# Performance work log

Measured on AMD Instinct MI355X. Metric: run time of the kernel, lower is better.

Reference implementation:

```python
import jax, jax.numpy as jnp
import numpy as np

SEQ_LEN = 2048
EMBED_DIM = 1024
NUM_HEADS = 16
DIM_HEAD = EMBED_DIM // NUM_HEADS
BATCH = 4


def setup_inputs() -> dict:
    key = jax.random.key(0)
    k1, k2, k3 = jax.random.split(key, 3)
    x = jax.random.normal(k1, (SEQ_LEN, BATCH, EMBED_DIM), dtype=jnp.float32)
    weight_qkv = jax.random.normal(k2, (3 * EMBED_DIM, EMBED_DIM), dtype=jnp.float32) * (EMBED_DIM ** -0.5)
    weight_out = jax.random.normal(k3, (EMBED_DIM, EMBED_DIM), dtype=jnp.float32) * (EMBED_DIM ** -0.5)
    # causal mask: True where attention is DISALLOWED (strict upper triangle)
    mask = ~jnp.tril(jnp.ones((SEQ_LEN, SEQ_LEN), dtype=bool))[None, None]  # [1,1,L,L]
    return {"x": x, "weight_qkv": weight_qkv, "weight_out": weight_out, "mask": mask}


def reference(x, weight_qkv, weight_out, mask):
    L, N, E = x.shape
    H, Dh = NUM_HEADS, DIM_HEAD
    scale = Dh ** -0.5
    qkv = x @ weight_qkv.T                       # [L, N, 3E]
    q, k, v = jnp.split(qkv, 3, axis=-1)         # each [L, N, E]
    # [L, N, E] -> [N*H, L, Dh]
    def to_heads(t):
        return t.reshape(L, N * H, Dh).transpose(1, 0, 2)
    q, k, v = to_heads(q) * scale, to_heads(k), to_heads(v)
    attn = jnp.einsum('bld,bmd->blm', q, k)      # [N*H, L, L]
    attn = attn.reshape(N, H, L, L)
    attn = jnp.where(mask, jnp.float32(-100000.0), attn)
    attn = jax.nn.softmax(attn.reshape(N * H, L, L), axis=-1)
    out = jnp.einsum('blm,bmd->bld', attn, v)    # [N*H, L, Dh]
    out = out.transpose(1, 0, 2).reshape(L, N, E)
    return out @ weight_out.T
```

## Files before the change

kernel.cpp:

```cpp
#include <hip/hip_runtime.h>
#include <hip/hip_bf16.h>
#include <stdint.h>

constexpr int L  = 2048;
constexpr int NB = 4;
constexpr int E  = 1024;
constexpr int H  = 16;
constexpr int M  = L * NB;
constexpr int K  = E;
constexpr int QKV_LD = 3 * E;

typedef float  f32x4  __attribute__((ext_vector_type(4)));
typedef float  f32x16 __attribute__((ext_vector_type(16)));
typedef __bf16 bf16x4 __attribute__((ext_vector_type(4)));
typedef __bf16 bf16x8 __attribute__((ext_vector_type(8)));
typedef unsigned int uint2v __attribute__((ext_vector_type(2)));
typedef unsigned int uint4v __attribute__((ext_vector_type(4)));

#define AS1 __attribute__((address_space(1)))
#define AS3 __attribute__((address_space(3)))

static __device__ __forceinline__ void gl_lds16(const void* g, void* l) {
  __builtin_amdgcn_global_load_lds((const AS1 uint32_t*)g, (AS3 uint32_t*)l, 16, 0, 0);
}

__global__ __launch_bounds__(256)
void cvt_all(const float* __restrict__ x, const float* __restrict__ wq,
             const float* __restrict__ wo, __bf16* __restrict__ xb,
             __bf16* __restrict__ wqb, __bf16* __restrict__ wob) {
  const int bid = blockIdx.x;
  const float* src;
  __bf16* dst;
  int i;
  if (bid < 8192)        { src = x;  dst = xb;  i = bid * 256 + threadIdx.x; }
  else if (bid < 11264)  { src = wq; dst = wqb; i = (bid - 8192) * 256 + threadIdx.x; }
  else                   { src = wo; dst = wob; i = (bid - 11264) * 256 + threadIdx.x; }
  const f32x4 v = ((const f32x4*)src)[i];
  bf16x4 o;
#pragma unroll
  for (int j = 0; j < 4; j++) o[j] = (__bf16)v[j];
  ((bf16x4*)dst)[i] = o;
}

template<int NC, typename OutT>
__global__ __launch_bounds__(256)
void gemm_bt(const __bf16* __restrict__ A, const __bf16* __restrict__ B,
             OutT* __restrict__ C) {
  constexpr int BK = 64;
  __shared__ char lds[2 * 128 * BK * 2];
  char* aL = lds;
  char* bL = lds + 128 * BK * 2;

  const int t    = threadIdx.x;
  const int lane = t & 63;
  const int w    = t >> 6;
  const int g    = lane >> 4;
  const int c    = lane & 15;

  const int nwg = gridDim.x * gridDim.y;
  const int lin = blockIdx.x + gridDim.x * blockIdx.y;
  const int q8  = nwg >> 3;
  const int swz = (lin & 7) * q8 + (lin >> 3);
  const int bx  = swz % gridDim.x;
  const int by  = swz / gridDim.x;

  const int rowBase = by * 128;
  const int colBase = bx * 128;

  const int srow = t >> 3;
  const int scb  = (t & 7) * 16;
  const int ssw  = scb ^ ((srow & 7) << 4);

  const char* aSrcBase = (const char*)(A + (size_t)(rowBase + srow) * K) + ssw;
  const char* bSrcBase = (const char*)(B + (size_t)(colBase + srow) * K) + ssw;

  f32x4 acc[4][4];
#pragma unroll
  for (int i = 0; i < 4; i++)
#pragma unroll
    for (int j = 0; j < 4; j++) acc[i][j] = f32x4{0.f, 0.f, 0.f, 0.f};

  const int wr = (w >> 1) * 64;
  const int wc = (w & 1) * 64;

  for (int k0 = 0; k0 < K; k0 += BK) {
    __syncthreads();
#pragma unroll
    for (int q = 0; q < 4; q++) {
      gl_lds16(aSrcBase + (size_t)2 * k0 + (size_t)q * 32 * K * 2, aL + q * 4096 + t * 16);
      gl_lds16(bSrcBase + (size_t)2 * k0 + (size_t)q * 32 * K * 2, bL + q * 4096 + t * 16);
    }
    __syncthreads();

    bf16x8 af[4][2], bfR[4][2];
#pragma unroll
    for (int mi = 0; mi < 4; mi++) {
      const int row = wr + mi * 16 + c;
      const int sw  = (row & 7) << 4;
#pragma unroll
      for (int ks = 0; ks < 2; ks++)
        af[mi][ks] = *(const bf16x8*)(aL + row * 128 + ((ks * 64 + g * 16) ^ sw));
    }
#pragma unroll
    for (int ni = 0; ni < 4; ni++) {
      const int row = wc + ni * 16 + c;
      const int sw  = (row & 7) << 4;
#pragma unroll
      for (int ks = 0; ks < 2; ks++)
        bfR[ni][ks] = *(const bf16x8*)(bL + row * 128 + ((ks * 64 + g * 16) ^ sw));
    }
#pragma unroll
    for (int mi = 0; mi < 4; mi++)
#pragma unroll
      for (int ni = 0; ni < 4; ni++)
#pragma unroll
        for (int ks = 0; ks < 2; ks++)
          acc[mi][ni] = __builtin_amdgcn_mfma_f32_16x16x32_bf16(
              af[mi][ks], bfR[ni][ks], acc[mi][ni], 0, 0, 0);
  }

#pragma unroll
  for (int mi = 0; mi < 4; mi++)
#pragma unroll
    for (int ni = 0; ni < 4; ni++)
#pragma unroll
      for (int r = 0; r < 4; r++) {
        const int row = rowBase + wr + mi * 16 + g * 4 + r;
        const int col = colBase + wc + ni * 16 + c;
        C[(size_t)row * NC + col] = (OutT)acc[mi][ni][r];
      }
}

__global__ __launch_bounds__(256)
void transpose_v(const __bf16* __restrict__ qkv, __bf16* __restrict__ vT) {
  __shared__ char tile[64 * 160];
  const int lt = blockIdx.x;
  const int bh = blockIdx.y;
  const int n  = bh >> 4, h = bh & 15;
  const int t  = threadIdx.x;
  const int r8 = t >> 3;
  const int c8 = (t & 7) * 8;

#pragma unroll
  for (int q2 = 0; q2 < 2; q2++) {
    const int l = q2 * 32 + r8;
    const bf16x8 v = *(const bf16x8*)(qkv + (size_t)((lt * 64 + l) * 4 + n) * QKV_LD +
                                      2 * E + h * 64 + c8);
    *(bf16x8*)(tile + l * 160 + ((c8 * 2) ^ (((l >> 3) & 7) << 4))) = v;
  }
  __syncthreads();
#pragma unroll
  for (int q2 = 0; q2 < 2; q2++) {
    const int d = q2 * 32 + r8;
    bf16x8 o;
#pragma unroll
    for (int i = 0; i < 8; i++) {
      const int l = c8 + i;
      o[i] = *(const __bf16*)(tile + l * 160 + ((d * 2) ^ (((l >> 3) & 7) << 4)));
    }
    *(bf16x8*)(vT + ((size_t)bh * 64 + d) * 2048 + lt * 64 + c8) = o;
  }
}

__global__ __launch_bounds__(256)
void attn_kernel(const __bf16* __restrict__ qkv, const __bf16* __restrict__ vT,
                 __bf16* __restrict__ out) {
  const int b  = blockIdx.x;
  const int y  = blockIdx.y;
  const int n  = b >> 4;
  const int h  = b & 15;

  __shared__ char kl[2][64 * 128];
  __shared__ char vl[2][64 * 128];

  const int t    = threadIdx.x;
  const int lane = t & 63;
  const int w    = t >> 6;
  const int l31  = lane & 31;
  const int hi   = lane >> 5;

  const int srow = t >> 3;
  const int scb  = (t & 7) * 16;
  int kssw[2];
#pragma unroll
  for (int q2 = 0; q2 < 2; q2++) {
    const int row = q2 * 32 + srow;
    kssw[q2] = scb ^ (((row ^ (row >> 3)) & 7) << 4);
  }

  const int krow0 = l31,      sw0 = ((krow0 ^ (krow0 >> 3)) & 7) << 4;
  const int krow1 = 32 + l31, sw1 = ((krow1 ^ (krow1 >> 3)) & 7) << 4;

  constexpr float QSCALE = 0.125f * 1.4426950408889634f;

  int cur = 0;

#pragma unroll
  for (int q2 = 0; q2 < 2; q2++) {
    const int kvrow = q2 * 32 + srow;
    gl_lds16((const char*)(qkv + (size_t)(kvrow * 4 + n) * QKV_LD + E + h * 64) + kssw[q2],
             kl[0] + q2 * 4096 + t * 16);
    gl_lds16((const char*)(vT + ((size_t)b * 64 + kvrow) * 2048) + kssw[q2],
             vl[0] + q2 * 4096 + t * 16);
  }

  for (int pass = 0; pass < 2; ++pass) {
    const int qsup = pass ? 15 - y : y;
    const int qb_  = qsup * 128 + w * 32;
    const int qg   = qb_ + l31;
    const int ktEnd = 2 * qsup + 1;

    bf16x8 qb[4];
    {
      const __bf16* qp = qkv + (size_t)(qg * 4 + n) * QKV_LD + h * 64;
#pragma unroll
      for (int ds = 0; ds < 4; ds++) {
        qb[ds] = *(const bf16x8*)(qp + ds * 16 + hi * 8);
#pragma unroll
        for (int i = 0; i < 8; i++) qb[ds][i] = (__bf16)((float)qb[ds][i] * QSCALE);
      }
    }

    float m_c = -3e38f, l_c = 0.f;
    f32x16 o0, o1;
#pragma unroll
    for (int j = 0; j < 16; j++) { o0[j] = 0.f; o1[j] = 0.f; }

    for (int kt = 0; kt <= ktEnd; ++kt) {
      __syncthreads();

      const bool last = (kt == ktEnd);
      if (!last || pass == 0) {
        const int nx = last ? 0 : kt + 1;
#pragma unroll
        for (int q2 = 0; q2 < 2; q2++) {
          const int kvrow = nx * 64 + q2 * 32 + srow;
          gl_lds16((const char*)(qkv + (size_t)(kvrow * 4 + n) * QKV_LD + E + h * 64) + kssw[q2],
                   kl[cur ^ 1] + q2 * 4096 + t * 16);
          const int vd = q2 * 32 + srow;
          gl_lds16((const char*)(vT + ((size_t)b * 64 + vd) * 2048 + nx * 64) + kssw[q2],
                   vl[cur ^ 1] + q2 * 4096 + t * 16);
        }
      }
      __builtin_amdgcn_sched_barrier(0);

      if (kt * 64 <= qb_ + 31) {
        const char* klc = kl[cur];
        const char* vlc = vl[cur];

        f32x16 s0, s1;
#pragma unroll
        for (int j = 0; j < 16; j++) { s0[j] = 0.f; s1[j] = 0.f; }
        __builtin_amdgcn_s_setprio(1);
#pragma unroll
        for (int ds = 0; ds < 4; ds++) {
          const int col = ds * 32 + hi * 16;
          const bf16x8 ka0 = *(const bf16x8*)(klc + krow0 * 128 + (col ^ sw0));
          const bf16x8 ka1 = *(const bf16x8*)(klc + krow1 * 128 + (col ^ sw1));
          s0 = __builtin_amdgcn_mfma_f32_32x32x16_bf16(ka0, qb[ds], s0, 0, 0, 0);
          s1 = __builtin_amdgcn_mfma_f32_32x32x16_bf16(ka1, qb[ds], s1, 0, 0, 0);
        }
        __builtin_amdgcn_s_setprio(0);

        if (kt * 64 + 63 > qb_) {
#pragma unroll
          for (int reg = 0; reg < 16; reg++) {
            const int kvp = (reg & 3) + 8 * (reg >> 2) + 4 * hi;
            if (kt * 64 + kvp      > qg) s0[reg] = -1e30f;
            if (kt * 64 + 32 + kvp > qg) s1[reg] = -1e30f;
          }
        }

        float rmax = s0[0];
#pragma unroll
        for (int reg = 1; reg < 16; reg++) rmax = fmaxf(rmax, s0[reg]);
#pragma unroll
        for (int reg = 0; reg < 16; reg++) rmax = fmaxf(rmax, s1[reg]);
        rmax = fmaxf(rmax, __shfl_xor(rmax, 32));

        if (__any(rmax > m_c + 8.f)) {
          const float mnew  = fmaxf(m_c, rmax);
          const float alpha = exp2f(m_c - mnew);
          l_c *= alpha;
#pragma unroll
          for (int reg = 0; reg < 16; reg++) {
            const int   qp = (reg & 3) + 8 * (reg >> 2) + 4 * hi;
            const float ar = __shfl(alpha, qp);
            o0[reg] *= ar;
            o1[reg] *= ar;
          }
          m_c = mnew;
        }

        float rsum = 0.f;
#pragma unroll
        for (int reg = 0; reg < 16; reg++) {
          const float e0 = exp2f(s0[reg] - m_c);
          const float e1 = exp2f(s1[reg] - m_c);
          s0[reg] = e0; s1[reg] = e1;
          rsum += e0 + e1;
        }
        rsum += __shfl_xor(rsum, 32);
        l_c += rsum;

        unsigned int runA[8], runB[8];
#pragma unroll
        for (int rg = 0; rg < 8; rg++) {
          bf16x4 pk;
#pragma unroll
          for (int j = 0; j < 4; j++)
            pk[j] = (__bf16)((rg < 4) ? s0[(rg & 3) * 4 + j] : s1[(rg & 3) * 4 + j]);
          const uint2v u = *(const uint2v*)&pk;
          runA[rg] = u[0]; runB[rg] = u[1];
        }

#pragma unroll
        for (int s_ = 0; s_ < 4; s_++) {
          const unsigned int ownA = hi ? runA[2 * s_ + 1] : runA[2 * s_];
          const unsigned int ownB = hi ? runB[2 * s_ + 1] : runB[2 * s_];
          const unsigned int sndA = hi ? runA[2 * s_]     : runA[2 * s_ + 1];
          const unsigned int sndB = hi ? runB[2 * s_]     : runB[2 * s_ + 1];
          const unsigned int rxA  = (unsigned int)__shfl_xor((int)sndA, 32);
          const unsigned int rxB  = (unsigned int)__shfl_xor((int)sndB, 32);
          uint4v pu;
          pu[0] = hi ? rxA : ownA;  pu[1] = hi ? rxB : ownB;
          pu[2] = hi ? ownA : rxA;  pu[3] = hi ? ownB : rxB;
          const bf16x8 pa = *(const bf16x8*)&pu;

          const int colp = s_ * 32 + hi * 16;
          const bf16x8 vb0 = *(const bf16x8*)(vlc + krow0 * 128 + (colp ^ sw0));
          const bf16x8 vb1 = *(const bf16x8*)(vlc + krow1 * 128 + (colp ^ sw1));
          __builtin_amdgcn_s_setprio(1);
          o0 = __builtin_amdgcn_mfma_f32_32x32x16_bf16(pa, vb0, o0, 0, 0, 0);
          o1 = __builtin_amdgcn_mfma_f32_32x32x16_bf16(pa, vb1, o1, 0, 0, 0);
          __builtin_amdgcn_s_setprio(0);
        }
      }

      cur ^= 1;
    }

    const float inv = 1.f / l_c;
#pragma unroll
    for (int reg = 0; reg < 16; reg++) {
      const int   qp  = (reg & 3) + 8 * (reg >> 2) + 4 * hi;
      const float li  = __shfl(inv, qp);
      const int   qrw = qb_ + qp;
      const size_t base = (size_t)(qrw * 4 + n) * E + h * 64;
      out[base + l31]      = (__bf16)(o0[reg] * li);
      out[base + 32 + l31] = (__bf16)(o1[reg] * li);
    }
  }
}

extern "C" void kernel_launch(void* const* d_in, const int* in_sizes, int n_in,
                              void* d_out, int out_size, void* d_ws, size_t ws_size,
                              hipStream_t stream) {
  const float* x    = (const float*)d_in[0];
  const float* wqkv = (const float*)d_in[1];
  const float* wout = (const float*)d_in[2];

  char* ws = (char*)d_ws;
  __bf16* x_bf    = (__bf16*)ws;                         ws += (size_t)M * E * 2;
  __bf16* wqkv_bf = (__bf16*)ws;                         ws += (size_t)QKV_LD * E * 2;
  __bf16* wout_bf = (__bf16*)ws;                         ws += (size_t)E * E * 2;
  __bf16* qkv     = (__bf16*)ws;                         ws += (size_t)M * QKV_LD * 2;
  __bf16* attno   = (__bf16*)ws;
  __bf16* vT      = x_bf;
  float*  outp    = (float*)d_out;

  cvt_all<<<12288, 256, 0, stream>>>(x, wqkv, wout, x_bf, wqkv_bf, wout_bf);

  gemm_bt<QKV_LD, __bf16><<<dim3(QKV_LD / 128, M / 128), 256, 0, stream>>>(x_bf, wqkv_bf, qkv);
  transpose_v<<<dim3(L / 64, NB * H), 256, 0, stream>>>(qkv, vT);
  attn_kernel<<<dim3(NB * H, 8), 256, 0, stream>>>(qkv, vT, attno);
  gemm_bt<E, float><<<dim3(E / 128, M / 128), 256, 0, stream>>>(attno, wout_bf, outp);
}
```

Before: 193.9 us.

## Split attention KV range across two warp groups with LDS merge of partial softmax

The attention block grows to 512 threads, forming two 4-wave groups that each cover part of the combined 34 KV-tile workload of the paired query blocks, 17 tiles per group. Group 1 finishes part of the long query block, saves its partial O, m and l to shared memory, then switches to the short block. Group 0 merges those partial results at the end. This balances work inside a block and doubles waves per block, but drops the double-buffered async prefetch in favour of load-then-sync each step. It also stores the partial O in bf16, which slightly reduces precision.

```diff
diff --git a/kernel.cpp b/kernel.cpp
--- a/kernel.cpp
+++ b/kernel.cpp
@@ -162,7 +162,7 @@
   }
 }
 
-__global__ __launch_bounds__(256)
+__global__ __launch_bounds__(512)
 void attn_kernel(const __bf16* __restrict__ qkv, const __bf16* __restrict__ vT,
                  __bf16* __restrict__ out) {
   const int b  = blockIdx.x;
@@ -170,17 +170,22 @@
   const int n  = b >> 4;
   const int h  = b & 15;
 
-  __shared__ char kl[2][64 * 128];
-  __shared__ char vl[2][64 * 128];
+  __shared__ char   kb[2][64 * 128];
+  __shared__ char   vb[2][64 * 128];
+  __shared__ __bf16 mO[128 * 64];
+  __shared__ float  mML[128 * 2];
 
   const int t    = threadIdx.x;
   const int lane = t & 63;
   const int w    = t >> 6;
+  const int wg   = w >> 2;
+  const int wl   = w & 3;
   const int l31  = lane & 31;
   const int hi   = lane >> 5;
 
-  const int srow = t >> 3;
-  const int scb  = (t & 7) * 16;
+  const int tg   = t & 255;
+  const int srow = tg >> 3;
+  const int scb  = (tg & 7) * 16;
   int kssw[2];
 #pragma unroll
   for (int q2 = 0; q2 < 2; q2++) {
@@ -193,153 +198,169 @@
 
   constexpr float QSCALE = 0.125f * 1.4426950408889634f;
 
-  int cur = 0;
-
-#pragma unroll
-  for (int q2 = 0; q2 < 2; q2++) {
-    const int kvrow = q2 * 32 + srow;
-    gl_lds16((const char*)(qkv + (size_t)(kvrow * 4 + n) * QKV_LD + E + h * 64) + kssw[q2],
-             kl[0] + q2 * 4096 + t * 16);
-    gl_lds16((const char*)(vT + ((size_t)b * 64 + kvrow) * 2048) + kssw[q2],
-             vl[0] + q2 * 4096 + t * 16);
-  }
-
-  for (int pass = 0; pass < 2; ++pass) {
-    const int qsup = pass ? 15 - y : y;
-    const int qb_  = qsup * 128 + w * 32;
-    const int qg   = qb_ + l31;
-    const int ktEnd = 2 * qsup + 1;
-
-    bf16x8 qb[4];
-    {
+  const int sS = y, sL = 15 - y;
+  const int jSwitch = 15 - 2 * y;
+
+  char* kls = kb[wg];
+  char* vls = vb[wg];
+
+  int qb_ = sL * 128 + wl * 32;
+  int qg  = qb_ + l31;
+
+  bf16x8 qf[4];
+  {
+    const __bf16* qp = qkv + (size_t)(qg * 4 + n) * QKV_LD + h * 64;
+#pragma unroll
+    for (int ds = 0; ds < 4; ds++) {
+      qf[ds] = *(const bf16x8*)(qp + ds * 16 + hi * 8);
+#pragma unroll
+      for (int i = 0; i < 8; i++) qf[ds][i] = (__bf16)((float)qf[ds][i] * QSCALE);
+    }
+  }
+
+  float m_c = -3e38f, l_c = 0.f;
+  f32x16 o0, o1;
+#pragma unroll
+  for (int j = 0; j < 16; j++) { o0[j] = 0.f; o1[j] = 0.f; }
+
+  for (int j = 0; j < 17; ++j) {
+    int kt;
+    if (wg == 0)            kt = j;
+    else if (j < jSwitch)   kt = 17 + j;
+    else                    kt = j - jSwitch;
+
+    if (wg == 1 && j == jSwitch) {
+#pragma unroll
+      for (int reg = 0; reg < 16; reg++) {
+        const int qp  = (reg & 3) + 8 * (reg >> 2) + 4 * hi;
+        const int row = wl * 32 + qp;
+        mO[row * 64 + l31]      = (__bf16)o0[reg];
+        mO[row * 64 + 32 + l31] = (__bf16)o1[reg];
+      }
+      if (hi == 0) {
+        mML[(wl * 32 + l31) * 2]     = m_c;
+        mML[(wl * 32 + l31) * 2 + 1] = l_c;
+      }
+      m_c = -3e38f; l_c = 0.f;
+#pragma unroll
+      for (int jj = 0; jj < 16; jj++) { o0[jj] = 0.f; o1[jj] = 0.f; }
+      qb_ = sS * 128 + wl * 32;
+      qg  = qb_ + l31;
       const __bf16* qp = qkv + (size_t)(qg * 4 + n) * QKV_LD + h * 64;
 #pragma unroll
       for (int ds = 0; ds < 4; ds++) {
-        qb[ds] = *(const bf16x8*)(qp + ds * 16 + hi * 8);
-#pragma unroll
-        for (int i = 0; i < 8; i++) qb[ds][i] = (__bf16)((float)qb[ds][i] * QSCALE);
-      }
-    }
-
-    float m_c = -3e38f, l_c = 0.f;
-    f32x16 o0, o1;
-#pragma unroll
-    for (int j = 0; j < 16; j++) { o0[j] = 0.f; o1[j] = 0.f; }
-
-    for (int kt = 0; kt <= ktEnd; ++kt) {
-      __syncthreads();
-
-      const bool last = (kt == ktEnd);
-      if (!last || pass == 0) {
-        const int nx = last ? 0 : kt + 1;
-#pragma unroll
-        for (int q2 = 0; q2 < 2; q2++) {
-          const int kvrow = nx * 64 + q2 * 32 + srow;
-          gl_lds16((const char*)(qkv + (size_t)(kvrow * 4 + n) * QKV_LD + E + h * 64) + kssw[q2],
-                   kl[cur ^ 1] + q2 * 4096 + t * 16);
-          const int vd = q2 * 32 + srow;
-          gl_lds16((const char*)(vT + ((size_t)b * 64 + vd) * 2048 + nx * 64) + kssw[q2],
-                   vl[cur ^ 1] + q2 * 4096 + t * 16);
+        qf[ds] = *(const bf16x8*)(qp + ds * 16 + hi * 8);
+#pragma unroll
+        for (int i = 0; i < 8; i++) qf[ds][i] = (__bf16)((float)qf[ds][i] * QSCALE);
+      }
+    }
+
+    __syncthreads();
+#pragma unroll
+    for (int q2 = 0; q2 < 2; q2++) {
+      const int kvrow = kt * 64 + q2 * 32 + srow;
+      gl_lds16((const char*)(qkv + (size_t)(kvrow * 4 + n) * QKV_LD + E + h * 64) + kssw[q2],
+               kls + q2 * 4096 + tg * 16);
+      const int vd = q2 * 32 + srow;
+      gl_lds16((const char*)(vT + ((size_t)b * 64 + vd) * 2048 + kt * 64) + kssw[q2],
+               vls + q2 * 4096 + tg * 16);
+    }
+    __syncthreads();
+
+    if (kt * 64 <= qb_ + 31) {
+      f32x16 s0, s1;
+#pragma unroll
+      for (int jj = 0; jj < 16; jj++) { s0[jj] = 0.f; s1[jj] = 0.f; }
+      __builtin_amdgcn_s_setprio(1);
+#pragma unroll
+      for (int ds = 0; ds < 4; ds++) {
+        const int col = ds * 32 + hi * 16;
+        const bf16x8 ka0 = *(const bf16x8*)(kls + krow0 * 128 + (col ^ sw0));
+        const bf16x8 ka1 = *(const bf16x8*)(kls + krow1 * 128 + (col ^ sw1));
+        s0 = __builtin_amdgcn_mfma_f32_32x32x16_bf16(ka0, qf[ds], s0, 0, 0, 0);
+        s1 = __builtin_amdgcn_mfma_f32_32x32x16_bf16(ka1, qf[ds], s1, 0, 0, 0);
+      }
+      __builtin_amdgcn_s_setprio(0);
+
+      if (kt * 64 + 63 > qb_) {
+#pragma unroll
+        for (int reg = 0; reg < 16; reg++) {
+          const int kvp = (reg & 3) + 8 * (reg >> 2) + 4 * hi;
+          if (kt * 64 + kvp      > qg) s0[reg] = -1e30f;
+          if (kt * 64 + 32 + kvp > qg) s1[reg] = -1e30f;
         }
       }
-      __builtin_amdgcn_sched_barrier(0);
-
-      if (kt * 64 <= qb_ + 31) {
-        const char* klc = kl[cur];
-        const char* vlc = vl[cur];
-
-        f32x16 s0, s1;
-#pragma unroll
-        for (int j = 0; j < 16; j++) { s0[j] = 0.f; s1[j] = 0.f; }
+
+      float rmax = s0[0];
+#pragma unroll
+      for (int reg = 1; reg < 16; reg++) rmax = fmaxf(rmax, s0[reg]);
+#pragma unroll
+      for (int reg = 0; reg < 16; reg++) rmax = fmaxf(rmax, s1[reg]);
+      rmax = fmaxf(rmax, __shfl_xor(rmax, 32));
+
+      if (__any(rmax > m_c + 8.f)) {
+        const float mnew  = fmaxf(m_c, rmax);
+        const float alpha = exp2f(m_c - mnew);
+        l_c *= alpha;
+#pragma unroll
+        for (int reg = 0; reg < 16; reg++) {
+          const int   qp = (reg & 3) + 8 * (reg >> 2) + 4 * hi;
+          const float ar = __shfl(alpha, qp);
+          o0[reg] *= ar;
+          o1[reg] *= ar;
+        }
+        m_c = mnew;
+      }
+
+      float rsum = 0.f;
+#pragma unroll
+      for (int reg = 0; reg < 16; reg++) {
+        const float e0 = exp2f(s0[reg] - m_c);
+        const float e1 = exp2f(s1[reg] - m_c);
+        s0[reg] = e0; s1[reg] = e1;
+        rsum += e0 + e1;
+      }
+      rsum += __shfl_xor(rsum, 32);
+      l_c += rsum;
+
+      unsigned int runA[8], runB[8];
+#pragma unroll
+      for (int rg = 0; rg < 8; rg++) {
+        bf16x4 pk;
+#pragma unroll
+        for (int jj = 0; jj < 4; jj++)
+          pk[jj] = (__bf16)((rg < 4) ? s0[(rg & 3) * 4 + jj] : s1[(rg & 3) * 4 + jj]);
+        const uint2v u = *(const uint2v*)&pk;
+        runA[rg] = u[0]; runB[rg] = u[1];
+      }
+
+#pragma unroll
+      for (int s_ = 0; s_ < 4; s_++) {
+        const unsigned int ownA = hi ? runA[2 * s_ + 1] : runA[2 * s_];
+        const unsigned int ownB = hi ? runB[2 * s_ + 1] : runB[2 * s_];
+        const unsigned int sndA = hi ? runA[2 * s_]     : runA[2 * s_ + 1];
+        const unsigned int sndB = hi ? runB[2 * s_]     : runB[2 * s_ + 1];
+        const unsigned int rxA  = (unsigned int)__shfl_xor((int)sndA, 32);
+        const unsigned int rxB  = (unsigned int)__shfl_xor((int)sndB, 32);
+        uint4v pu;
+        pu[0] = hi ? rxA : ownA;  pu[1] = hi ? rxB : ownB;
+        pu[2] = hi ? ownA : rxA;  pu[3] = hi ? ownB : rxB;
+        const bf16x8 pa = *(const bf16x8*)&pu;
+
+        const int colp = s_ * 32 + hi * 16;
+        const bf16x8 vb0 = *(const bf16x8*)(vls + krow0 * 128 + (colp ^ sw0));
+        const bf16x8 vb1 = *(const bf16x8*)(vls + krow1 * 128 + (colp ^ sw1));
         __builtin_amdgcn_s_setprio(1);
-#pragma unroll
-        for (int ds = 0; ds < 4; ds++) {
-          const int col = ds * 32 + hi * 16;
-          const bf16x8 ka0 = *(const bf16x8*)(klc + krow0 * 128 + (col ^ sw0));
-          const bf16x8 ka1 = *(const bf16x8*)(klc + krow1 * 128 + (col ^ sw1));
-          s0 = __builtin_amdgcn_mfma_f32_32x32x16_bf16(ka0, qb[ds], s0, 0, 0, 0);
-          s1 = __builtin_amdgcn_mfma_f32_32x32x16_bf16(ka1, qb[ds], s1, 0, 0, 0);
-        }
+        o0 = __builtin_amdgcn_mfma_f32_32x32x16_bf16(pa, vb0, o0, 0, 0, 0);
+        o1 = __builtin_amdgcn_mfma_f32_32x32x16_bf16(pa, vb1, o1, 0, 0, 0);
         __builtin_amdgcn_s_setprio(0);
-
-        if (kt * 64 + 63 > qb_) {
-#pragma unroll
-          for (int reg = 0; reg < 16; reg++) {
-            const int kvp = (reg & 3) + 8 * (reg >> 2) + 4 * hi;
-            if (kt * 64 + kvp      > qg) s0[reg] = -1e30f;
-            if (kt * 64 + 32 + kvp > qg) s1[reg] = -1e30f;
-          }
-        }
-
-        float rmax = s0[0];
-#pragma unroll
-        for (int reg = 1; reg < 16; reg++) rmax = fmaxf(rmax, s0[reg]);
-#pragma unroll
-        for (int reg = 0; reg < 16; reg++) rmax = fmaxf(rmax, s1[reg]);
-        rmax = fmaxf(rmax, __shfl_xor(rmax, 32));
-
-        if (__any(rmax > m_c + 8.f)) {
-          const float mnew  = fmaxf(m_c, rmax);
-          const float alpha = exp2f(m_c - mnew);
-          l_c *= alpha;
-#pragma unroll
-          for (int reg = 0; reg < 16; reg++) {
-            const int   qp = (reg & 3) + 8 * (reg >> 2) + 4 * hi;
-            const float ar = __shfl(alpha, qp);
-            o0[reg] *= ar;
-            o1[reg] *= ar;
-          }
-          m_c = mnew;
-        }
-
-        float rsum = 0.f;
-#pragma unroll
-        for (int reg = 0; reg < 16; reg++) {
-          const float e0 = exp2f(s0[reg] - m_c);
-          const float e1 = exp2f(s1[reg] - m_c);
-          s0[reg] = e0; s1[reg] = e1;
-          rsum += e0 + e1;
-        }
-        rsum += __shfl_xor(rsum, 32);
-        l_c += rsum;
-
-        unsigned int runA[8], runB[8];
-#pragma unroll
-        for (int rg = 0; rg < 8; rg++) {
-          bf16x4 pk;
-#pragma unroll
-          for (int j = 0; j < 4; j++)
-            pk[j] = (__bf16)((rg < 4) ? s0[(rg & 3) * 4 + j] : s1[(rg & 3) * 4 + j]);
-          const uint2v u = *(const uint2v*)&pk;
-          runA[rg] = u[0]; runB[rg] = u[1];
-        }
-
-#pragma unroll
-        for (int s_ = 0; s_ < 4; s_++) {
-          const unsigned int ownA = hi ? runA[2 * s_ + 1] : runA[2 * s_];
-          const unsigned int ownB = hi ? runB[2 * s_ + 1] : runB[2 * s_];
-          const unsigned int sndA = hi ? runA[2 * s_]     : runA[2 * s_ + 1];
-          const unsigned int sndB = hi ? runB[2 * s_]     : runB[2 * s_ + 1];
-          const unsigned int rxA  = (unsigned int)__shfl_xor((int)sndA, 32);
-          const unsigned int rxB  = (unsigned int)__shfl_xor((int)sndB, 32);
-          uint4v pu;
-          pu[0] = hi ? rxA : ownA;  pu[1] = hi ? rxB : ownB;
-          pu[2] = hi ? ownA : rxA;  pu[3] = hi ? ownB : rxB;
-          const bf16x8 pa = *(const bf16x8*)&pu;
-
-          const int colp = s_ * 32 + hi * 16;
-          const bf16x8 vb0 = *(const bf16x8*)(vlc + krow0 * 128 + (colp ^ sw0));
-          const bf16x8 vb1 = *(const bf16x8*)(vlc + krow1 * 128 + (colp ^ sw1));
-          __builtin_amdgcn_s_setprio(1);
-          o0 = __builtin_amdgcn_mfma_f32_32x32x16_bf16(pa, vb0, o0, 0, 0, 0);
-          o1 = __builtin_amdgcn_mfma_f32_32x32x16_bf16(pa, vb1, o1, 0, 0, 0);
-          __builtin_amdgcn_s_setprio(0);
-        }
-      }
-
-      cur ^= 1;
-    }
-
+      }
+    }
+  }
+
+  __syncthreads();
+
+  if (wg == 1) {
     const float inv = 1.f / l_c;
 #pragma unroll
     for (int reg = 0; reg < 16; reg++) {
@@ -349,6 +370,30 @@
       const size_t base = (size_t)(qrw * 4 + n) * E + h * 64;
       out[base + l31]      = (__bf16)(o0[reg] * li);
       out[base + 32 + l31] = (__bf16)(o1[reg] * li);
+    }
+  } else {
+    const float mB = mML[(wl * 32 + l31) * 2];
+    const float lB = mML[(wl * 32 + l31) * 2 + 1];
+    const float mF = fmaxf(m_c, mB);
+    const float aA = exp2f(m_c - mF);
+    const float aB = exp2f(mB - mF);
+    const float lF = l_c * aA + lB * aB;
+    const float iv = 1.f / lF;
+#pragma unroll
+    for (int reg = 0; reg < 16; reg++) {
+      const int   qp  = (reg & 3) + 8 * (reg >> 2) + 4 * hi;
+      const float aAr = __shfl(aA, qp);
+      const float aBr = __shfl(aB, qp);
+      const float ivr = __shfl(iv, qp);
+      const int   row = wl * 32 + qp;
+      const float b0  = (float)mO[row * 64 + l31];
+      const float b1  = (float)mO[row * 64 + 32 + l31];
+      const float v0  = (o0[reg] * aAr + b0 * aBr) * ivr;
+      const float v1  = (o1[reg] * aAr + b1 * aBr) * ivr;
+      const int   qrw = qb_ + qp;
+      const size_t base = (size_t)(qrw * 4 + n) * E + h * 64;
+      out[base + l31]      = (__bf16)v0;
+      out[base + 32 + l31] = (__bf16)v1;
     }
   }
 }
@@ -373,6 +418,6 @@
 
   gemm_bt<QKV_LD, __bf16><<<dim3(QKV_LD / 128, M / 128), 256, 0, stream>>>(x_bf, wqkv_bf, qkv);
   transpose_v<<<dim3(L / 64, NB * H), 256, 0, stream>>>(qkv, vT);
-  attn_kernel<<<dim3(NB * H, 8), 256, 0, stream>>>(qkv, vT, attno);
+  attn_kernel<<<dim3(NB * H, 8), 512, 0, stream>>>(qkv, vT, attno);
   gemm_bt<E, float><<<dim3(E / 128, M / 128), 256, 0, stream>>>(attno, wout_bf, outp);
 }
```

New measurement: 197.8 us. No clear change (+2.0%).

## Double KV tile size to 128 in causal attention kernel

Applied to the files above, without the earlier changes.

The attention kernel now processes 128 keys/values per iteration instead of 64, using four score accumulators per wave and a wider V tile with matching swizzles. This halves the number of loop iterations and barriers and amortizes softmax bookkeeping, but doubles LDS usage and register pressure. It also drops the per-wave skip of fully masked tiles, so on the diagonal tile some waves compute fully masked blocks.

```diff
diff --git a/kernel.cpp b/kernel.cpp
--- a/kernel.cpp
+++ b/kernel.cpp
@@ -170,8 +170,8 @@
   const int n  = b >> 4;
   const int h  = b & 15;
 
-  __shared__ char kl[2][64 * 128];
-  __shared__ char vl[2][64 * 128];
+  __shared__ char kl[2][128 * 128];
+  __shared__ char vl[2][64 * 256];
 
   const int t    = threadIdx.x;
   const int lane = t & 63;
@@ -179,28 +179,44 @@
   const int l31  = lane & 31;
   const int hi   = lane >> 5;
 
-  const int srow = t >> 3;
-  const int scb  = (t & 7) * 16;
-  int kssw[2];
-#pragma unroll
-  for (int q2 = 0; q2 < 2; q2++) {
-    const int row = q2 * 32 + srow;
-    kssw[q2] = scb ^ (((row ^ (row >> 3)) & 7) << 4);
-  }
-
-  const int krow0 = l31,      sw0 = ((krow0 ^ (krow0 >> 3)) & 7) << 4;
-  const int krow1 = 32 + l31, sw1 = ((krow1 ^ (krow1 >> 3)) & 7) << 4;
+  const int srowK = t >> 3;
+  const int scbK  = (t & 7) * 16;
+  int sswK[4];
+#pragma unroll
+  for (int q2 = 0; q2 < 4; q2++) {
+    const int row = q2 * 32 + srowK;
+    sswK[q2] = scbK ^ (((row ^ (row >> 3)) & 7) << 4);
+  }
+  const int srowV = t >> 4;
+  const int scbV  = (t & 15) * 16;
+  int sswV[4];
+#pragma unroll
+  for (int q2 = 0; q2 < 4; q2++) {
+    const int row = q2 * 16 + srowV;
+    sswV[q2] = scbV ^ (((row ^ (row >> 3)) & 7) << 4);
+  }
+
+  int ksw[4];
+#pragma unroll
+  for (int j = 0; j < 4; j++) {
+    const int row = j * 32 + l31;
+    ksw[j] = ((row ^ (row >> 3)) & 7) << 4;
+  }
+  const int vsw0 = ((l31 ^ (l31 >> 3)) & 7) << 4;
+  const int vrow1 = 32 + l31;
+  const int vsw1 = ((vrow1 ^ (vrow1 >> 3)) & 7) << 4;
 
   constexpr float QSCALE = 0.125f * 1.4426950408889634f;
 
   int cur = 0;
 
 #pragma unroll
-  for (int q2 = 0; q2 < 2; q2++) {
-    const int kvrow = q2 * 32 + srow;
-    gl_lds16((const char*)(qkv + (size_t)(kvrow * 4 + n) * QKV_LD + E + h * 64) + kssw[q2],
+  for (int q2 = 0; q2 < 4; q2++) {
+    const int kvrow = q2 * 32 + srowK;
+    gl_lds16((const char*)(qkv + (size_t)(kvrow * 4 + n) * QKV_LD + E + h * 64) + sswK[q2],
              kl[0] + q2 * 4096 + t * 16);
-    gl_lds16((const char*)(vT + ((size_t)b * 64 + kvrow) * 2048) + kssw[q2],
+    const int vd = q2 * 16 + srowV;
+    gl_lds16((const char*)(vT + ((size_t)b * 64 + vd) * 2048) + sswV[q2],
              vl[0] + q2 * 4096 + t * 16);
   }
 
@@ -208,7 +224,7 @@
     const int qsup = pass ? 15 - y : y;
     const int qb_  = qsup * 128 + w * 32;
     const int qg   = qb_ + l31;
-    const int ktEnd = 2 * qsup + 1;
+    const int ktEnd = qsup;
 
     bf16x8 qb[4];
     {
@@ -233,108 +249,129 @@
       if (!last || pass == 0) {
         const int nx = last ? 0 : kt + 1;
 #pragma unroll
-        for (int q2 = 0; q2 < 2; q2++) {
-          const int kvrow = nx * 64 + q2 * 32 + srow;
-          gl_lds16((const char*)(qkv + (size_t)(kvrow * 4 + n) * QKV_LD + E + h * 64) + kssw[q2],
+        for (int q2 = 0; q2 < 4; q2++) {
+          const int kvrow = nx * 128 + q2 * 32 + srowK;
+          gl_lds16((const char*)(qkv + (size_t)(kvrow * 4 + n) * QKV_LD + E + h * 64) + sswK[q2],
                    kl[cur ^ 1] + q2 * 4096 + t * 16);
-          const int vd = q2 * 32 + srow;
-          gl_lds16((const char*)(vT + ((size_t)b * 64 + vd) * 2048 + nx * 64) + kssw[q2],
+          const int vd = q2 * 16 + srowV;
+          gl_lds16((const char*)(vT + ((size_t)b * 64 + vd) * 2048 + nx * 128) + sswV[q2],
                    vl[cur ^ 1] + q2 * 4096 + t * 16);
         }
       }
       __builtin_amdgcn_sched_barrier(0);
 
-      if (kt * 64 <= qb_ + 31) {
-        const char* klc = kl[cur];
-        const char* vlc = vl[cur];
-
-        f32x16 s0, s1;
-#pragma unroll
-        for (int j = 0; j < 16; j++) { s0[j] = 0.f; s1[j] = 0.f; }
+      const char* klc = kl[cur];
+      const char* vlc = vl[cur];
+
+      f32x16 s0, s1, s2, s3;
+#pragma unroll
+      for (int j = 0; j < 16; j++) { s0[j] = 0.f; s1[j] = 0.f; s2[j] = 0.f; s3[j] = 0.f; }
+      __builtin_amdgcn_s_setprio(1);
+#pragma unroll
+      for (int ds = 0; ds < 4; ds++) {
+        const int col = ds * 32 + hi * 16;
+        const bf16x8 ka0 = *(const bf16x8*)(klc + (0 * 32 + l31) * 128 + (col ^ ksw[0]));
+        const bf16x8 ka1 = *(const bf16x8*)(klc + (1 * 32 + l31) * 128 + (col ^ ksw[1]));
+        const bf16x8 ka2 = *(const bf16x8*)(klc + (2 * 32 + l31) * 128 + (col ^ ksw[2]));
+        const bf16x8 ka3 = *(const bf16x8*)(klc + (3 * 32 + l31) * 128 + (col ^ ksw[3]));
+        s0 = __builtin_amdgcn_mfma_f32_32x32x16_bf16(ka0, qb[ds], s0, 0, 0, 0);
+        s1 = __builtin_amdgcn_mfma_f32_32x32x16_bf16(ka1, qb[ds], s1, 0, 0, 0);
+        s2 = __builtin_amdgcn_mfma_f32_32x32x16_bf16(ka2, qb[ds], s2, 0, 0, 0);
+        s3 = __builtin_amdgcn_mfma_f32_32x32x16_bf16(ka3, qb[ds], s3, 0, 0, 0);
+      }
+      __builtin_amdgcn_s_setprio(0);
+
+      if (last) {
+#pragma unroll
+        for (int reg = 0; reg < 16; reg++) {
+          const int kvp = (reg & 3) + 8 * (reg >> 2) + 4 * hi;
+          const int kb0 = kt * 128 + kvp;
+          if (kb0      > qg) s0[reg] = -1e30f;
+          if (kb0 + 32 > qg) s1[reg] = -1e30f;
+          if (kb0 + 64 > qg) s2[reg] = -1e30f;
+          if (kb0 + 96 > qg) s3[reg] = -1e30f;
+        }
+      }
+
+      float rmax = s0[0];
+#pragma unroll
+      for (int reg = 1; reg < 16; reg++) rmax = fmaxf(rmax, s0[reg]);
+#pragma unroll
+      for (int reg = 0; reg < 16; reg++) rmax = fmaxf(rmax, s1[reg]);
+#pragma unroll
+      for (int reg = 0; reg < 16; reg++) rmax = fmaxf(rmax, s2[reg]);
+#pragma unroll
+      for (int reg = 0; reg < 16; reg++) rmax = fmaxf(rmax, s3[reg]);
+      rmax = fmaxf(rmax, __shfl_xor(rmax, 32));
+
+      if (__any(rmax > m_c + 8.f)) {
+        const float mnew  = fmaxf(m_c, rmax);
+        const float alpha = exp2f(m_c - mnew);
+        l_c *= alpha;
+#pragma unroll
+        for (int reg = 0; reg < 16; reg++) {
+          const int   qp = (reg & 3) + 8 * (reg >> 2) + 4 * hi;
+          const float ar = __shfl(alpha, qp);
+          o0[reg] *= ar;
+          o1[reg] *= ar;
+        }
+        m_c = mnew;
+      }
+
+      float rsum = 0.f;
+#pragma unroll
+      for (int reg = 0; reg < 16; reg++) {
+        const float e0 = exp2f(s0[reg] - m_c);
+        const float e1 = exp2f(s1[reg] - m_c);
+        const float e2 = exp2f(s2[reg] - m_c);
+        const float e3 = exp2f(s3[reg] - m_c);
+        s0[reg] = e0; s1[reg] = e1; s2[reg] = e2; s3[reg] = e3;
+        rsum += (e0 + e1) + (e2 + e3);
+      }
+      rsum += __shfl_xor(rsum, 32);
+      l_c += rsum;
+
+      unsigned int runA[16], runB[16];
+#pragma unroll
+      for (int f = 0; f < 4; f++)
+#pragma unroll
+        for (int rg = 0; rg < 4; rg++) {
+          bf16x4 pk;
+#pragma unroll
+          for (int j = 0; j < 4; j++) {
+            const int r = rg * 4 + j;
+            float v;
+            if      (f == 0) v = s0[r];
+            else if (f == 1) v = s1[r];
+            else if (f == 2) v = s2[r];
+            else             v = s3[r];
+            pk[j] = (__bf16)v;
+          }
+          const uint2v u = *(const uint2v*)&pk;
+          runA[f * 4 + rg] = u[0]; runB[f * 4 + rg] = u[1];
+        }
+
+#pragma unroll
+      for (int s_ = 0; s_ < 8; s_++) {
+        const int rg0 = (s_ >> 1) * 4 + 2 * (s_ & 1);
+        const unsigned int ownA = hi ? runA[rg0 + 1] : runA[rg0];
+        const unsigned int ownB = hi ? runB[rg0 + 1] : runB[rg0];
+        const unsigned int sndA = hi ? runA[rg0]     : runA[rg0 + 1];
+        const unsigned int sndB = hi ? runB[rg0]     : runB[rg0 + 1];
+        const unsigned int rxA  = (unsigned int)__shfl_xor((int)sndA, 32);
+        const unsigned int rxB  = (unsigned int)__shfl_xor((int)sndB, 32);
+        uint4v pu;
+        pu[0] = hi ? rxA : ownA;  pu[1] = hi ? rxB : ownB;
+        pu[2] = hi ? ownA : rxA;  pu[3] = hi ? ownB : rxB;
+        const bf16x8 pa = *(const bf16x8*)&pu;
+
+        const int colp = s_ * 32 + hi * 16;
+        const bf16x8 vb0 = *(const bf16x8*)(vlc + l31 * 256 + (colp ^ vsw0));
+        const bf16x8 vb1 = *(const bf16x8*)(vlc + vrow1 * 256 + (colp ^ vsw1));
         __builtin_amdgcn_s_setprio(1);
-#pragma unroll
-        for (int ds = 0; ds < 4; ds++) {
-          const int col = ds * 32 + hi * 16;
-          const bf16x8 ka0 = *(const bf16x8*)(klc + krow0 * 128 + (col ^ sw0));
-          const bf16x8 ka1 = *(const bf16x8*)(klc + krow1 * 128 + (col ^ sw1));
-          s0 = __builtin_amdgcn_mfma_f32_32x32x16_bf16(ka0, qb[ds], s0, 0, 0, 0);
-          s1 = __builtin_amdgcn_mfma_f32_32x32x16_bf16(ka1, qb[ds], s1, 0, 0, 0);
-        }
+        o0 = __builtin_amdgcn_mfma_f32_32x32x16_bf16(pa, vb0, o0, 0, 0, 0);
+        o1 = __builtin_amdgcn_mfma_f32_32x32x16_bf16(pa, vb1, o1, 0, 0, 0);
         __builtin_amdgcn_s_setprio(0);
-
-        if (kt * 64 + 63 > qb_) {
-#pragma unroll
-          for (int reg = 0; reg < 16; reg++) {
-            const int kvp = (reg & 3) + 8 * (reg >> 2) + 4 * hi;
-            if (kt * 64 + kvp      > qg) s0[reg] = -1e30f;
-            if (kt * 64 + 32 + kvp > qg) s1[reg] = -1e30f;
-          }
-        }
-
-        float rmax = s0[0];
-#pragma unroll
-        for (int reg = 1; reg < 16; reg++) rmax = fmaxf(rmax, s0[reg]);
-#pragma unroll
-        for (int reg = 0; reg < 16; reg++) rmax = fmaxf(rmax, s1[reg]);
-        rmax = fmaxf(rmax, __shfl_xor(rmax, 32));
-
-        if (__any(rmax > m_c + 8.f)) {
-          const float mnew  = fmaxf(m_c, rmax);
-          const float alpha = exp2f(m_c - mnew);
-          l_c *= alpha;
-#pragma unroll
-          for (int reg = 0; reg < 16; reg++) {
-            const int   qp = (reg & 3) + 8 * (reg >> 2) + 4 * hi;
-            const float ar = __shfl(alpha, qp);
-            o0[reg] *= ar;
-            o1[reg] *= ar;
-          }
-          m_c = mnew;
-        }
-
-        float rsum = 0.f;
-#pragma unroll
-        for (int reg = 0; reg < 16; reg++) {
-          const float e0 = exp2f(s0[reg] - m_c);
-          const float e1 = exp2f(s1[reg] - m_c);
-          s0[reg] = e0; s1[reg] = e1;
-          rsum += e0 + e1;
-        }
-        rsum += __shfl_xor(rsum, 32);
-        l_c += rsum;
-
-        unsigned int runA[8], runB[8];
-#pragma unroll
-        for (int rg = 0; rg < 8; rg++) {
-          bf16x4 pk;
-#pragma unroll
-          for (int j = 0; j < 4; j++)
-            pk[j] = (__bf16)((rg < 4) ? s0[(rg & 3) * 4 + j] : s1[(rg & 3) * 4 + j]);
-          const uint2v u = *(const uint2v*)&pk;
-          runA[rg] = u[0]; runB[rg] = u[1];
-        }
-
-#pragma unroll
-        for (int s_ = 0; s_ < 4; s_++) {
-          const unsigned int ownA = hi ? runA[2 * s_ + 1] : runA[2 * s_];
-          const unsigned int ownB = hi ? runB[2 * s_ + 1] : runB[2 * s_];
-          const unsigned int sndA = hi ? runA[2 * s_]     : runA[2 * s_ + 1];
-          const unsigned int sndB = hi ? runB[2 * s_]     : runB[2 * s_ + 1];
-          const unsigned int rxA  = (unsigned int)__shfl_xor((int)sndA, 32);
-          const unsigned int rxB  = (unsigned int)__shfl_xor((int)sndB, 32);
-          uint4v pu;
-          pu[0] = hi ? rxA : ownA;  pu[1] = hi ? rxB : ownB;
-          pu[2] = hi ? ownA : rxA;  pu[3] = hi ? ownB : rxB;
-          const bf16x8 pa = *(const bf16x8*)&pu;
-
-          const int colp = s_ * 32 + hi * 16;
-          const bf16x8 vb0 = *(const bf16x8*)(vlc + krow0 * 128 + (colp ^ sw0));
-          const bf16x8 vb1 = *(const bf16x8*)(vlc + krow1 * 128 + (colp ^ sw1));
-          __builtin_amdgcn_s_setprio(1);
-          o0 = __builtin_amdgcn_mfma_f32_32x32x16_bf16(pa, vb0, o0, 0, 0, 0);
-          o1 = __builtin_amdgcn_mfma_f32_32x32x16_bf16(pa, vb1, o1, 0, 0, 0);
-          __builtin_amdgcn_s_setprio(0);
-        }
       }
 
       cur ^= 1;
```

After: 214.3 us. +10.5%, slower.

## Split attention into 64-row query blocks with 2 waves, drop double-buffering

Applied to the files above, without the earlier changes.

Restructures the attention kernel from 8 blocks per head (256 threads, 128-row query tiles, paired light/heavy passes for causal balance) into 32 blocks per head of 128 threads, each handling a single 64-row query tile. The grid is launched heaviest-first so long causal rows start early. K/V tiles are now loaded single-buffered with a sync on each side instead of being prefetched into a double buffer. The aim is more blocks and occupancy on the GPU and less shared memory per block. The cost is exposed load latency on every tile and K/V reloaded by more blocks.

```diff
diff --git a/kernel.cpp b/kernel.cpp
--- a/kernel.cpp
+++ b/kernel.cpp
@@ -162,16 +162,16 @@
   }
 }
 
-__global__ __launch_bounds__(256)
+__global__ __launch_bounds__(128)
 void attn_kernel(const __bf16* __restrict__ qkv, const __bf16* __restrict__ vT,
                  __bf16* __restrict__ out) {
-  const int b  = blockIdx.x;
-  const int y  = blockIdx.y;
-  const int n  = b >> 4;
-  const int h  = b & 15;
-
-  __shared__ char kl[2][64 * 128];
-  __shared__ char vl[2][64 * 128];
+  const int b   = blockIdx.x;
+  const int sup = 31 - (int)blockIdx.y;
+  const int n   = b >> 4;
+  const int h   = b & 15;
+
+  __shared__ char kl[64 * 128];
+  __shared__ char vl[64 * 128];
 
   const int t    = threadIdx.x;
   const int lane = t & 63;
@@ -181,10 +181,10 @@
 
   const int srow = t >> 3;
   const int scb  = (t & 7) * 16;
-  int kssw[2];
-#pragma unroll
-  for (int q2 = 0; q2 < 2; q2++) {
-    const int row = q2 * 32 + srow;
+  int kssw[4];
+#pragma unroll
+  for (int q2 = 0; q2 < 4; q2++) {
+    const int row = q2 * 16 + srow;
     kssw[q2] = scb ^ (((row ^ (row >> 3)) & 7) << 4);
   }
 
@@ -193,163 +193,136 @@
 
   constexpr float QSCALE = 0.125f * 1.4426950408889634f;
 
-  int cur = 0;
-
-#pragma unroll
-  for (int q2 = 0; q2 < 2; q2++) {
-    const int kvrow = q2 * 32 + srow;
-    gl_lds16((const char*)(qkv + (size_t)(kvrow * 4 + n) * QKV_LD + E + h * 64) + kssw[q2],
-             kl[0] + q2 * 4096 + t * 16);
-    gl_lds16((const char*)(vT + ((size_t)b * 64 + kvrow) * 2048) + kssw[q2],
-             vl[0] + q2 * 4096 + t * 16);
-  }
-
-  for (int pass = 0; pass < 2; ++pass) {
-    const int qsup = pass ? 15 - y : y;
-    const int qb_  = qsup * 128 + w * 32;
-    const int qg   = qb_ + l31;
-    const int ktEnd = 2 * qsup + 1;
-
-    bf16x8 qb[4];
-    {
-      const __bf16* qp = qkv + (size_t)(qg * 4 + n) * QKV_LD + h * 64;
-#pragma unroll
-      for (int ds = 0; ds < 4; ds++) {
-        qb[ds] = *(const bf16x8*)(qp + ds * 16 + hi * 8);
-#pragma unroll
-        for (int i = 0; i < 8; i++) qb[ds][i] = (__bf16)((float)qb[ds][i] * QSCALE);
+  const int qb_ = sup * 64 + w * 32;
+  const int qg  = qb_ + l31;
+
+  bf16x8 qb[4];
+  {
+    const __bf16* qp = qkv + (size_t)(qg * 4 + n) * QKV_LD + h * 64;
+#pragma unroll
+    for (int ds = 0; ds < 4; ds++) {
+      qb[ds] = *(const bf16x8*)(qp + ds * 16 + hi * 8);
+#pragma unroll
+      for (int i = 0; i < 8; i++) qb[ds][i] = (__bf16)((float)qb[ds][i] * QSCALE);
+    }
+  }
+
+  float m_c = -3e38f, l_c = 0.f;
+  f32x16 o0, o1;
+#pragma unroll
+  for (int j = 0; j < 16; j++) { o0[j] = 0.f; o1[j] = 0.f; }
+
+  for (int kt = 0; kt <= sup; ++kt) {
+    __syncthreads();
+#pragma unroll
+    for (int q2 = 0; q2 < 4; q2++) {
+      const int kvrow = kt * 64 + q2 * 16 + srow;
+      gl_lds16((const char*)(qkv + (size_t)(kvrow * 4 + n) * QKV_LD + E + h * 64) + kssw[q2],
+               kl + q2 * 2048 + t * 16);
+      const int vd = q2 * 16 + srow;
+      gl_lds16((const char*)(vT + ((size_t)b * 64 + vd) * 2048 + kt * 64) + kssw[q2],
+               vl + q2 * 2048 + t * 16);
+    }
+    __syncthreads();
+
+    f32x16 s0, s1;
+#pragma unroll
+    for (int j = 0; j < 16; j++) { s0[j] = 0.f; s1[j] = 0.f; }
+    __builtin_amdgcn_s_setprio(1);
+#pragma unroll
+    for (int ds = 0; ds < 4; ds++) {
+      const int col = ds * 32 + hi * 16;
+      const bf16x8 ka0 = *(const bf16x8*)(kl + krow0 * 128 + (col ^ sw0));
+      const bf16x8 ka1 = *(const bf16x8*)(kl + krow1 * 128 + (col ^ sw1));
+      s0 = __builtin_amdgcn_mfma_f32_32x32x16_bf16(ka0, qb[ds], s0, 0, 0, 0);
+      s1 = __builtin_amdgcn_mfma_f32_32x32x16_bf16(ka1, qb[ds], s1, 0, 0, 0);
+    }
+    __builtin_amdgcn_s_setprio(0);
+
+    if (kt == sup) {
+#pragma unroll
+      for (int reg = 0; reg < 16; reg++) {
+        const int kvp = (reg & 3) + 8 * (reg >> 2) + 4 * hi;
+        if (kt * 64 + kvp      > qg) s0[reg] = -1e30f;
+        if (kt * 64 + 32 + kvp > qg) s1[reg] = -1e30f;
       }
     }
 
-    float m_c = -3e38f, l_c = 0.f;
-    f32x16 o0, o1;
-#pragma unroll
-    for (int j = 0; j < 16; j++) { o0[j] = 0.f; o1[j] = 0.f; }
-
-    for (int kt = 0; kt <= ktEnd; ++kt) {
-      __syncthreads();
-
-      const bool last = (kt == ktEnd);
-      if (!last || pass == 0) {
-        const int nx = last ? 0 : kt + 1;
-#pragma unroll
-        for (int q2 = 0; q2 < 2; q2++) {
-          const int kvrow = nx * 64 + q2 * 32 + srow;
-          gl_lds16((const char*)(qkv + (size_t)(kvrow * 4 + n) * QKV_LD + E + h * 64) + kssw[q2],
-                   kl[cur ^ 1] + q2 * 4096 + t * 16);
-          const int vd = q2 * 32 + srow;
-          gl_lds16((const char*)(vT + ((size_t)b * 64 + vd) * 2048 + nx * 64) + kssw[q2],
-                   vl[cur ^ 1] + q2 * 4096 + t * 16);
-        }
+    float rmax = s0[0];
+#pragma unroll
+    for (int reg = 1; reg < 16; reg++) rmax = fmaxf(rmax, s0[reg]);
+#pragma unroll
+    for (int reg = 0; reg < 16; reg++) rmax = fmaxf(rmax, s1[reg]);
+    rmax = fmaxf(rmax, __shfl_xor(rmax, 32));
+
+    if (__any(rmax > m_c + 8.f)) {
+      const float mnew  = fmaxf(m_c, rmax);
+      const float alpha = exp2f(m_c - mnew);
+      l_c *= alpha;
+#pragma unroll
+      for (int reg = 0; reg < 16; reg++) {
+        const int   qp = (reg & 3) + 8 * (reg >> 2) + 4 * hi;
+        const float ar = __shfl(alpha, qp);
+        o0[reg] *= ar;
+        o1[reg] *= ar;
       }
-      __builtin_amdgcn_sched_barrier(0);
-
-      if (kt * 64 <= qb_ + 31) {
-        const char* klc = kl[cur];
-        const char* vlc = vl[cur];
-
-        f32x16 s0, s1;
-#pragma unroll
-        for (int j = 0; j < 16; j++) { s0[j] = 0.f; s1[j] = 0.f; }
-        __builtin_amdgcn_s_setprio(1);
-#pragma unroll
-        for (int ds = 0; ds < 4; ds++) {
-          const int col = ds * 32 + hi * 16;
-          const bf16x8 ka0 = *(const bf16x8*)(klc + krow0 * 128 + (col ^ sw0));
-          const bf16x8 ka1 = *(const bf16x8*)(klc + krow1 * 128 + (col ^ sw1));
-          s0 = __builtin_amdgcn_mfma_f32_32x32x16_bf16(ka0, qb[ds], s0, 0, 0, 0);
-          s1 = __builtin_amdgcn_mfma_f32_32x32x16_bf16(ka1, qb[ds], s1, 0, 0, 0);
-        }
-        __builtin_amdgcn_s_setprio(0);
-
-        if (kt * 64 + 63 > qb_) {
-#pragma unroll
-          for (int reg = 0; reg < 16; reg++) {
-            const int kvp = (reg & 3) + 8 * (reg >> 2) + 4 * hi;
-            if (kt * 64 + kvp      > qg) s0[reg] = -1e30f;
-            if (kt * 64 + 32 + kvp > qg) s1[reg] = -1e30f;
-          }
-        }
-
-        float rmax = s0[0];
-#pragma unroll
-        for (int reg = 1; reg < 16; reg++) rmax = fmaxf(rmax, s0[reg]);
-#pragma unroll
-        for (int reg = 0; reg < 16; reg++) rmax = fmaxf(rmax, s1[reg]);
-        rmax = fmaxf(rmax, __shfl_xor(rmax, 32));
-
-        if (__any(rmax > m_c + 8.f)) {
-          const float mnew  = fmaxf(m_c, rmax);
-          const float alpha = exp2f(m_c - mnew);
-          l_c *= alpha;
-#pragma unroll
-          for (int reg = 0; reg < 16; reg++) {
-            const int   qp = (reg & 3) + 8 * (reg >> 2) + 4 * hi;
-            const float ar = __shfl(alpha, qp);
-            o0[reg] *= ar;
-            o1[reg] *= ar;
-          }
-          m_c = mnew;
-        }
-
-        float rsum = 0.f;
-#pragma unroll
-        for (int reg = 0; reg < 16; reg++) {
-          const float e0 = exp2f(s0[reg] - m_c);
-          const float e1 = exp2f(s1[reg] - m_c);
-          s0[reg] = e0; s1[reg] = e1;
-          rsum += e0 + e1;
-        }
-        rsum += __shfl_xor(rsum, 32);
-        l_c += rsum;
-
-        unsigned int runA[8], runB[8];
-#pragma unroll
-        for (int rg = 0; rg < 8; rg++) {
-          bf16x4 pk;
-#pragma unroll
-          for (int j = 0; j < 4; j++)
-            pk[j] = (__bf16)((rg < 4) ? s0[(rg & 3) * 4 + j] : s1[(rg & 3) * 4 + j]);
-          const uint2v u = *(const uint2v*)&pk;
-          runA[rg] = u[0]; runB[rg] = u[1];
-        }
-
-#pragma unroll
-        for (int s_ = 0; s_ < 4; s_++) {
-          const unsigned int ownA = hi ? runA[2 * s_ + 1] : runA[2 * s_];
-          const unsigned int ownB = hi ? runB[2 * s_ + 1] : runB[2 * s_];
-          const unsigned int sndA = hi ? runA[2 * s_]     : runA[2 * s_ + 1];
-          const unsigned int sndB = hi ? runB[2 * s_]     : runB[2 * s_ + 1];
-          const unsigned int rxA  = (unsigned int)__shfl_xor((int)sndA, 32);
-          const unsigned int rxB  = (unsigned int)__shfl_xor((int)sndB, 32);
-          uint4v pu;
-          pu[0] = hi ? rxA : ownA;  pu[1] = hi ? rxB : ownB;
-          pu[2] = hi ? ownA : rxA;  pu[3] = hi ? ownB : rxB;
-          const bf16x8 pa = *(const bf16x8*)&pu;
-
-          const int colp = s_ * 32 + hi * 16;
-          const bf16x8 vb0 = *(const bf16x8*)(vlc + krow0 * 128 + (colp ^ sw0));
-          const bf16x8 vb1 = *(const bf16x8*)(vlc + krow1 * 128 + (colp ^ sw1));
-          __builtin_amdgcn_s_setprio(1);
-          o0 = __builtin_amdgcn_mfma_f32_32x32x16_bf16(pa, vb0, o0, 0, 0, 0);
-          o1 = __builtin_amdgcn_mfma_f32_32x32x16_bf16(pa, vb1, o1, 0, 0, 0);
-          __builtin_amdgcn_s_setprio(0);
-        }
-      }
-
-      cur ^= 1;
-    }
-
-    const float inv = 1.f / l_c;
+      m_c = mnew;
+    }
+
+    float rsum = 0.f;
 #pragma unroll
     for (int reg = 0; reg < 16; reg++) {
-      const int   qp  = (reg & 3) + 8 * (reg >> 2) + 4 * hi;
-      const float li  = __shfl(inv, qp);
-      const int   qrw = qb_ + qp;
-      const size_t base = (size_t)(qrw * 4 + n) * E + h * 64;
-      out[base + l31]      = (__bf16)(o0[reg] * li);
-      out[base + 32 + l31] = (__bf16)(o1[reg] * li);
-    }
+      const float e0 = exp2f(s0[reg] - m_c);
+      const float e1 = exp2f(s1[reg] - m_c);
+      s0[reg] = e0; s1[reg] = e1;
+      rsum += e0 + e1;
+    }
+    rsum += __shfl_xor(rsum, 32);
+    l_c += rsum;
+
+    unsigned int runA[8], runB[8];
+#pragma unroll
+    for (int rg = 0; rg < 8; rg++) {
+      bf16x4 pk;
+#pragma unroll
+      for (int j = 0; j < 4; j++)
+        pk[j] = (__bf16)((rg < 4) ? s0[(rg & 3) * 4 + j] : s1[(rg & 3) * 4 + j]);
+      const uint2v u = *(const uint2v*)&pk;
+      runA[rg] = u[0]; runB[rg] = u[1];
+    }
+
+#pragma unroll
+    for (int s_ = 0; s_ < 4; s_++) {
+      const unsigned int ownA = hi ? runA[2 * s_ + 1] : runA[2 * s_];
+      const unsigned int ownB = hi ? runB[2 * s_ + 1] : runB[2 * s_];
+      const unsigned int sndA = hi ? runA[2 * s_]     : runA[2 * s_ + 1];
+      const unsigned int sndB = hi ? runB[2 * s_]     : runB[2 * s_ + 1];
+      const unsigned int rxA  = (unsigned int)__shfl_xor((int)sndA, 32);
+      const unsigned int rxB  = (unsigned int)__shfl_xor((int)sndB, 32);
+      uint4v pu;
+      pu[0] = hi ? rxA : ownA;  pu[1] = hi ? rxB : ownB;
+      pu[2] = hi ? ownA : rxA;  pu[3] = hi ? ownB : rxB;
+      const bf16x8 pa = *(const bf16x8*)&pu;
+
+      const int colp = s_ * 32 + hi * 16;
+      const bf16x8 vb0 = *(const bf16x8*)(vl + krow0 * 128 + (colp ^ sw0));
+      const bf16x8 vb1 = *(const bf16x8*)(vl + krow1 * 128 + (colp ^ sw1));
+      __builtin_amdgcn_s_setprio(1);
+      o0 = __builtin_amdgcn_mfma_f32_32x32x16_bf16(pa, vb0, o0, 0, 0, 0);
+      o1 = __builtin_amdgcn_mfma_f32_32x32x16_bf16(pa, vb1, o1, 0, 0, 0);
+      __builtin_amdgcn_s_setprio(0);
+    }
+  }
+
+  const float inv = 1.f / l_c;
+#pragma unroll
+  for (int reg = 0; reg < 16; reg++) {
+    const int   qp  = (reg & 3) + 8 * (reg >> 2) + 4 * hi;
+    const float li  = __shfl(inv, qp);
+    const int   qrw = qb_ + qp;
+    const size_t base = (size_t)(qrw * 4 + n) * E + h * 64;
+    out[base + l31]      = (__bf16)(o0[reg] * li);
+    out[base + 32 + l31] = (__bf16)(o1[reg] * li);
   }
 }
 
@@ -373,6 +346,6 @@
 
   gemm_bt<QKV_LD, __bf16><<<dim3(QKV_LD / 128, M / 128), 256, 0, stream>>>(x_bf, wqkv_bf, qkv);
   transpose_v<<<dim3(L / 64, NB * H), 256, 0, stream>>>(qkv, vT);
-  attn_kernel<<<dim3(NB * H, 8), 256, 0, stream>>>(qkv, vT, attno);
+  attn_kernel<<<dim3(NB * H, 32), 128, 0, stream>>>(qkv, vT, attno);
   gemm_bt<E, float><<<dim3(E / 128, M / 128), 256, 0, stream>>>(attno, wout_bf, outp);
 }
```

After: 192.8 us, median of 2. No clear change (-0.6%).
